# Kernel tuning notes

Measured on AMD Instinct MI355X. Metric: run time of the kernel, lower is better.

## Reference

```python
import jax, jax.numpy as jnp
import numpy as np

B, S, HID = 2, 2048, 4096
H, KVH, D = 32, 8, 128
EPS = 1e-6
BASE = 1000000.0


def _rmsnorm(x, w, eps=EPS):
    # x: [..., D]; RMSNorm over last dim with learned scale
    return x * jax.lax.rsqrt(jnp.mean(x * x, axis=-1, keepdims=True) + eps) * w


def _rope_interleaved(x, cos, sin):
    # x: [B, S, h, D]; cos/sin: [S, D//2]; is_neox_style=False (GPT-J interleaved pairs)
    x1 = x[..., 0::2]
    x2 = x[..., 1::2]
    c = cos[None, :, None, :]
    s = sin[None, :, None, :]
    o1 = x1 * c - x2 * s
    o2 = x2 * c + x1 * s
    return jnp.stack([o1, o2], axis=-1).reshape(x.shape)


def setup_inputs() -> dict:
    key = jax.random.key(0)
    ks = jax.random.split(key, 6)
    scale = 0.02
    return {
        "positions": jnp.arange(S, dtype=jnp.int32),
        "hidden_states": jax.random.normal(ks[0], (B, S, HID), jnp.float32),
        "Wq": jax.random.normal(ks[1], (HID, H * D), jnp.float32) * scale,
        "Wk": jax.random.normal(ks[2], (HID, KVH * D), jnp.float32) * scale,
        "Wv": jax.random.normal(ks[3], (HID, KVH * D), jnp.float32) * scale,
        "Wo": jax.random.normal(ks[4], (H * D, HID), jnp.float32) * scale,
        "q_norm_w": jnp.ones((D,), jnp.float32),
        "k_norm_w": jnp.ones((D,), jnp.float32),
    }


def reference(positions, hidden_states, Wq, Wk, Wv, Wo, q_norm_w, k_norm_w):
    # QKV projections (no bias)
    q = hidden_states @ Wq            # [B,S,H*D]
    k = hidden_states @ Wk            # [B,S,KVH*D]
    v = hidden_states @ Wv            # [B,S,KVH*D]

    # per-head QK RMSNorm
    q = _rmsnorm(q.reshape(B, S, H, D), q_norm_w)
    k = _rmsnorm(k.reshape(B, S, KVH, D), k_norm_w)
    v = v.reshape(B, S, KVH, D)

    # RoPE (non-neox / interleaved), rotary_dim == head_dim
    inv_freq = BASE ** (-jnp.arange(0, D, 2, dtype=jnp.float32) / D)  # [D/2]
    freqs = positions.astype(jnp.float32)[:, None] * inv_freq[None, :]  # [S, D/2]
    cos, sin = jnp.cos(freqs), jnp.sin(freqs)
    q = _rope_interleaved(q, cos, sin)
    k = _rope_interleaved(k, cos, sin)

    # GQA causal attention (prefill path of RadixAttention)
    rep = H // KVH
    kr = jnp.repeat(k, rep, axis=2)   # [B,S,H,D]
    vr = jnp.repeat(v, rep, axis=2)
    scores = jnp.einsum("bqhd,bkhd->bhqk", q, kr) * (D ** -0.5)
    causal = jnp.tril(jnp.ones((S, S), dtype=bool))
    scores = jnp.where(causal[None, None], scores, jnp.float32(-1e30))
    probs = jax.nn.softmax(scores, axis=-1)
    attn = jnp.einsum("bhqk,bkhd->bqhd", probs, vr).reshape(B, S, H * D)

    out = attn @ Wo                   # [B,S,HID]
    return out, k.reshape(B, S, KVH * D), v.reshape(B, S, KVH * D)
```

## Files before the change

### kernel.cpp

```cpp
#include <hip/hip_runtime.h>
#include <math.h>

#define B_SZ 2
#define S_LEN 2048
#define HID_D 4096
#define NH 32
#define NKV 8
#define HD 128
#define NTOK (B_SZ * S_LEN)

typedef short bf16x8 __attribute__((ext_vector_type(8)));
typedef float f32x4 __attribute__((ext_vector_type(4)));

__device__ inline unsigned short bf_rn(float f) {
    unsigned int u = __builtin_bit_cast(unsigned int, f);
    return (unsigned short)((u + 0x7FFFu + ((u >> 16) & 1u)) >> 16);
}
__device__ inline float bf_up(unsigned short s) {
    return __builtin_bit_cast(float, (unsigned int)s << 16);
}

__device__ inline void gload_lds16(const void* g, void* l) {
    __builtin_amdgcn_global_load_lds(
        (const __attribute__((address_space(1))) unsigned int*)g,
        (__attribute__((address_space(3))) unsigned int*)l, 16, 0, 0);
}

__global__ __launch_bounds__(64) void rope_table_kernel(const int* __restrict__ pos,
                                                        float* __restrict__ cosT,
                                                        float* __restrict__ sinT) {
    int s = blockIdx.x;
    int i = threadIdx.x;
    float p = (float)pos[s];
    float inv = expf((float)i * (-13.815510557964274f / 64.0f));
    float f = p * inv;
    cosT[s * 64 + i] = cosf(f);
    sinT[s * 64 + i] = sinf(f);
}

__global__ __launch_bounds__(256) void castv_kernel(const float* __restrict__ src,
                                                    unsigned short* __restrict__ dst,
                                                    int nquads) {
    int i = blockIdx.x * 256 + threadIdx.x;
    if (i >= nquads) return;
    float4 v = ((const float4*)src)[i];
    ushort4 o;
    o.x = bf_rn(v.x); o.y = bf_rn(v.y); o.z = bf_rn(v.z); o.w = bf_rn(v.w);
    ((ushort4*)dst)[i] = o;
}

__global__ __launch_bounds__(256) void cast_t_kernel(const float* __restrict__ src,
                                                     unsigned short* __restrict__ dst,
                                                     int K, int N) {
    __shared__ float tile[32][33];
    const int j0 = blockIdx.x << 5;
    const int i0 = blockIdx.y << 5;
    const int tx = threadIdx.x & 31, ty = threadIdx.x >> 5;
#pragma unroll
    for (int r = 0; r < 32; r += 8)
        tile[ty + r][tx] = src[(size_t)(i0 + ty + r) * N + j0 + tx];
    __syncthreads();
#pragma unroll
    for (int r = 0; r < 32; r += 8)
        dst[(size_t)(j0 + ty + r) * K + i0 + tx] = bf_rn(tile[tx][ty + r]);
}

__global__ __launch_bounds__(256) void vtrans_kernel(const float* __restrict__ vout,
                                                     unsigned short* __restrict__ vtb) {
    __shared__ float tile[32][33];
    const int bh = blockIdx.z;
    const int s0 = blockIdx.x << 5;
    const int d0 = blockIdx.y << 5;
    const int b = bh >> 3, kvh = bh & 7;
    const int tx = threadIdx.x & 31, ty = threadIdx.x >> 5;
#pragma unroll
    for (int r = 0; r < 32; r += 8)
        tile[ty + r][tx] = vout[((size_t)(b * S_LEN + s0 + ty + r) * NKV + kvh) * HD + d0 + tx];
    __syncthreads();
#pragma unroll
    for (int r = 0; r < 32; r += 8)
        vtb[((size_t)(b * NKV + kvh) * HD + d0 + ty + r) * S_LEN + s0 + tx] = bf_rn(tile[tx][ty + r]);
}

template <typename OUT>
__global__ __launch_bounds__(256) void gemm_bt_kernel(const unsigned short* __restrict__ A,
                                                      const unsigned short* __restrict__ Bt,
                                                      OUT* __restrict__ C,
                                                      int M, int N, int K) {
    __shared__ unsigned short As[128 * 32];
    __shared__ unsigned short Bs[128 * 32];
    const int t = threadIdx.x;
    const int lane = t & 63, w = t >> 6;
    const int wr = w >> 1, wc = w & 1;
    const int bm = blockIdx.y << 7, bn = blockIdx.x << 7;

    const int srow = w * 32 + (lane >> 2);
    const int skoff = (lane & 3) << 3;
    const unsigned short* aA0 = A + (size_t)(bm + srow) * K + skoff;
    const unsigned short* aA1 = aA0 + (size_t)16 * K;
    const unsigned short* aB0 = Bt + (size_t)(bn + srow) * K + skoff;
    const unsigned short* aB1 = aB0 + (size_t)16 * K;
    unsigned short* lA0 = As + (w * 2 + 0) * 512;
    unsigned short* lA1 = As + (w * 2 + 1) * 512;
    unsigned short* lB0 = Bs + (w * 2 + 0) * 512;
    unsigned short* lB1 = Bs + (w * 2 + 1) * 512;

    const int fr = lane & 15, fg = lane >> 4;
    const unsigned short* Asp = As + (wr * 64 + fr) * 32 + fg * 8;
    const unsigned short* Bsp = Bs + (wc * 64 + fr) * 32 + fg * 8;

    f32x4 acc[4][4];
#pragma unroll
    for (int m = 0; m < 4; ++m)
#pragma unroll
        for (int n = 0; n < 4; ++n) acc[m][n] = (f32x4)(0.0f);

    const int nk = K >> 5;
    for (int kc = 0; kc < nk; ++kc) {
        __syncthreads();
        const size_t go = (size_t)kc * 32;
        gload_lds16(aA0 + go, lA0);
        gload_lds16(aA1 + go, lA1);
        gload_lds16(aB0 + go, lB0);
        gload_lds16(aB1 + go, lB1);
        __syncthreads();

        bf16x8 af[4], bfr[4];
#pragma unroll
        for (int m = 0; m < 4; ++m) af[m] = *(const bf16x8*)(Asp + m * 512);
#pragma unroll
        for (int n = 0; n < 4; ++n) bfr[n] = *(const bf16x8*)(Bsp + n * 512);
#pragma unroll
        for (int m = 0; m < 4; ++m)
#pragma unroll
            for (int n = 0; n < 4; ++n)
                acc[m][n] = __builtin_amdgcn_mfma_f32_16x16x32_bf16(af[m], bfr[n], acc[m][n], 0, 0, 0);
    }

    const int crow = (lane >> 4) << 2, ccol = lane & 15;
#pragma unroll
    for (int m = 0; m < 4; ++m)
#pragma unroll
        for (int n = 0; n < 4; ++n) {
            OUT* Cp = C + (size_t)(bm + wr * 64 + m * 16 + crow) * N + bn + wc * 64 + n * 16 + ccol;
#pragma unroll
            for (int r = 0; r < 4; ++r) {
                float v = acc[m][n][r];
                if constexpr (sizeof(OUT) == 2) Cp[(size_t)r * N] = bf_rn(v);
                else                            Cp[(size_t)r * N] = v;
            }
        }
}

__global__ __launch_bounds__(64) void norm_rope_kernel(float* __restrict__ buf,
                                                       const float* __restrict__ w,
                                                       const float* __restrict__ cosT,
                                                       const float* __restrict__ sinT,
                                                       int nh) {
    int bid = blockIdx.x;
    int token = bid / nh;
    int h = bid - token * nh;
    int pos = token & (S_LEN - 1);
    int i = threadIdx.x;
    size_t base = (size_t)token * (nh * HD) + (size_t)h * HD + 2 * i;
    float2 x = *(const float2*)(buf + base);
    float ss = x.x * x.x + x.y * x.y;
#pragma unroll
    for (int off = 32; off > 0; off >>= 1) ss += __shfl_xor(ss, off);
    float rn = 1.0f / sqrtf(ss * (1.0f / 128.0f) + 1e-6f);
    float2 wv = *(const float2*)(w + 2 * i);
    float x1 = x.x * rn * wv.x;
    float x2 = x.y * rn * wv.y;
    float c = cosT[pos * 64 + i];
    float sn = sinT[pos * 64 + i];
    float2 o;
    o.x = x1 * c - x2 * sn;
    o.y = x2 * c + x1 * sn;
    *(float2*)(buf + base) = o;
}

__global__ __launch_bounds__(64) void norm_rope_bf16_kernel(unsigned short* __restrict__ buf,
                                                            const float* __restrict__ w,
                                                            const float* __restrict__ cosT,
                                                            const float* __restrict__ sinT,
                                                            int nh) {
    int bid = blockIdx.x;
    int token = bid / nh;
    int h = bid - token * nh;
    int pos = token & (S_LEN - 1);
    int i = threadIdx.x;
    size_t base = (size_t)token * (nh * HD) + (size_t)h * HD + 2 * i;
    unsigned int u = *(const unsigned int*)(buf + base);
    float x1 = bf_up((unsigned short)(u & 0xFFFFu));
    float x2 = bf_up((unsigned short)(u >> 16));
    float ss = x1 * x1 + x2 * x2;
#pragma unroll
    for (int off = 32; off > 0; off >>= 1) ss += __shfl_xor(ss, off);
    float rn = 1.0f / sqrtf(ss * (1.0f / 128.0f) + 1e-6f);
    float2 wv = *(const float2*)(w + 2 * i);
    x1 *= rn * wv.x;
    x2 *= rn * wv.y;
    float c = cosT[pos * 64 + i];
    float sn = sinT[pos * 64 + i];
    float o1 = x1 * c - x2 * sn;
    float o2 = x2 * c + x1 * sn;
    unsigned int ou = (unsigned int)bf_rn(o1) | ((unsigned int)bf_rn(o2) << 16);
    *(unsigned int*)(buf + base) = ou;
}

#define PADQ 136
#define PADV 72

__global__ __launch_bounds__(256) void attn_mfma_kernel(const unsigned short* __restrict__ Qb,
                                                        const float* __restrict__ Kf,
                                                        const unsigned short* __restrict__ Vb,
                                                        unsigned short* __restrict__ O) {
    __shared__ unsigned short Qs[64 * PADQ];
    __shared__ unsigned short Ks[64 * PADQ];
    __shared__ unsigned short Vt[128 * PADV];
    __shared__ unsigned short Ps[64 * PADV];
    const int t = threadIdx.x;
    const int lane = t & 63, w = t >> 6;
    const int c = lane & 15, g = lane >> 4;
    const int qt = blockIdx.x, h = blockIdx.y, b = blockIdx.z;
    const int kvh = h >> 2;
    const size_t tok0 = (size_t)b * S_LEN + (size_t)qt * 64;
    const size_t vbase = ((size_t)(b * NKV + kvh)) * HD * S_LEN;

    {
        const int r = t >> 2, c0 = (t & 3) * 32;
        const uint4* src = (const uint4*)(Qb + (tok0 + r) * HID_D + (size_t)h * HD + c0);
        uint4* dst = (uint4*)(Qs + r * PADQ + c0);
#pragma unroll
        for (int j = 0; j < 4; ++j) dst[j] = src[j];
    }
    __syncthreads();

    bf16x8 qf[4];
    {
        const unsigned short* qp = Qs + (w * 16 + c) * PADQ + g * 8;
#pragma unroll
        for (int ks = 0; ks < 4; ++ks) qf[ks] = *(const bf16x8*)(qp + ks * 32);
    }

    f32x4 o[8];
#pragma unroll
    for (int dt = 0; dt < 8; ++dt) o[dt] = (f32x4)(0.0f);
    float mrow[4], lrow[4];
#pragma unroll
    for (int r = 0; r < 4; ++r) { mrow[r] = -INFINITY; lrow[r] = 0.0f; }
    const float sc = 0.12751743f;

    for (int kt = 0; kt <= qt; ++kt) {
        __syncthreads();
        {
            const int r = t >> 2, c0 = (t & 3) * 32;
            const size_t gbase = ((size_t)b * S_LEN + (size_t)kt * 64 + r) * (NKV * HD) + (size_t)kvh * HD + c0;
            unsigned short* kd = Ks + r * PADQ + c0;
#pragma unroll
            for (int j = 0; j < 8; ++j) {
                float4 v = *(const float4*)(Kf + gbase + j * 4);
                ushort4 o4;
                o4.x = bf_rn(v.x); o4.y = bf_rn(v.y); o4.z = bf_rn(v.z); o4.w = bf_rn(v.w);
                *(ushort4*)(kd + j * 4) = o4;
            }
            const int vr = t >> 3;
            const int vc8 = (t & 7) * 8;
            const unsigned short* vsrc = Vb + vbase + (size_t)kt * 64 + vc8;
#pragma unroll
            for (int pp = 0; pp < 4; ++pp) {
                const int d = vr + pp * 32;
                *(uint4*)(Vt + d * PADV + vc8) = *(const uint4*)(vsrc + (size_t)d * S_LEN);
            }
        }
        __syncthreads();

        f32x4 s[4];
#pragma unroll
        for (int ct = 0; ct < 4; ++ct) s[ct] = (f32x4)(0.0f);
#pragma unroll
        for (int ks = 0; ks < 4; ++ks) {
            bf16x8 kf[4];
#pragma unroll
            for (int ct = 0; ct < 4; ++ct)
                kf[ct] = *(const bf16x8*)(Ks + (ct * 16 + c) * PADQ + ks * 32 + g * 8);
#pragma unroll
            for (int ct = 0; ct < 4; ++ct)
                s[ct] = __builtin_amdgcn_mfma_f32_16x16x32_bf16(qf[ks], kf[ct], s[ct], 0, 0, 0);
        }

        const int rowbase = qt * 64 + w * 16 + g * 4;
        const int colbase = kt * 64 + c;
#pragma unroll
        for (int r = 0; r < 4; ++r) {
            float v0 = s[0][r] * sc, v1 = s[1][r] * sc, v2 = s[2][r] * sc, v3 = s[3][r] * sc;
            if (kt == qt) {
                const int rq = rowbase + r;
                if (colbase + 0  > rq) v0 = -1e30f;
                if (colbase + 16 > rq) v1 = -1e30f;
                if (colbase + 32 > rq) v2 = -1e30f;
                if (colbase + 48 > rq) v3 = -1e30f;
            }
            float mx = fmaxf(fmaxf(v0, v1), fmaxf(v2, v3));
#pragma unroll
            for (int off = 8; off > 0; off >>= 1) mx = fmaxf(mx, __shfl_xor(mx, off));
            const float mn = fmaxf(mrow[r], mx);
            const float sf = exp2f(mrow[r] - mn);
            mrow[r] = mn;
            const float p0 = exp2f(v0 - mn), p1 = exp2f(v1 - mn);
            const float p2 = exp2f(v2 - mn), p3 = exp2f(v3 - mn);
            unsigned short* pr = Ps + (w * 16 + g * 4 + r) * PADV + c;
            pr[0]  = bf_rn(p0);
            pr[16] = bf_rn(p1);
            pr[32] = bf_rn(p2);
            pr[48] = bf_rn(p3);
            float rs = p0 + p1 + p2 + p3;
#pragma unroll
            for (int off = 8; off > 0; off >>= 1) rs += __shfl_xor(rs, off);
            lrow[r] = lrow[r] * sf + rs;
#pragma unroll
            for (int dt = 0; dt < 8; ++dt) o[dt][r] *= sf;
        }

#pragma unroll
        for (int ks = 0; ks < 2; ++ks) {
            bf16x8 pf = *(const bf16x8*)(Ps + (w * 16 + c) * PADV + ks * 32 + g * 8);
#pragma unroll
            for (int dt = 0; dt < 8; ++dt) {
                bf16x8 vf = *(const bf16x8*)(Vt + (dt * 16 + c) * PADV + ks * 32 + g * 8);
                o[dt] = __builtin_amdgcn_mfma_f32_16x16x32_bf16(pf, vf, o[dt], 0, 0, 0);
            }
        }
    }

#pragma unroll
    for (int r = 0; r < 4; ++r) {
        const float inv = 1.0f / lrow[r];
        const size_t rowoff = (tok0 + w * 16 + g * 4 + r) * HID_D + (size_t)h * HD;
#pragma unroll
        for (int dt = 0; dt < 8; ++dt)
            O[rowoff + dt * 16 + c] = bf_rn(o[dt][r] * inv);
    }
}

extern "C" void kernel_launch(void* const* d_in, const int* in_sizes, int n_in,
                              void* d_out, int out_size, void* d_ws, size_t ws_size,
                              hipStream_t stream) {
    const int* positions = (const int*)d_in[0];
    const float* hidden  = (const float*)d_in[1];
    const float* Wq      = (const float*)d_in[2];
    const float* Wk      = (const float*)d_in[3];
    const float* Wv      = (const float*)d_in[4];
    const float* Wo      = (const float*)d_in[5];
    const float* qw      = (const float*)d_in[6];
    const float* kw      = (const float*)d_in[7];

    float* out  = (float*)d_out;
    float* kout = out + (size_t)NTOK * HID_D;
    float* vout = kout + (size_t)NTOK * NKV * HD;

    char* w8 = (char*)d_ws;
    float* cosT = (float*)w8;
    float* sinT = cosT + S_LEN * 64;
    unsigned short* qbuf = (unsigned short*)(sinT + S_LEN * 64);
    unsigned short* hb   = qbuf + (size_t)NTOK * HID_D;
    unsigned short* Wt   = hb + (size_t)NTOK * HID_D;
    unsigned short* vtb  = Wt + (size_t)HID_D * HID_D;
    unsigned short* ab   = hb;

    rope_table_kernel<<<S_LEN, 64, 0, stream>>>(positions, cosT, sinT);
    castv_kernel<<<(NTOK * HID_D / 4 + 255) / 256, 256, 0, stream>>>(hidden, hb, NTOK * HID_D / 4);

    cast_t_kernel<<<dim3(NKV * HD / 32, HID_D / 32), 256, 0, stream>>>(Wk, Wt, HID_D, NKV * HD);
    gemm_bt_kernel<float><<<dim3(NKV * HD / 128, NTOK / 128), 256, 0, stream>>>(hb, Wt, kout, NTOK, NKV * HD, HID_D);
    cast_t_kernel<<<dim3(NKV * HD / 32, HID_D / 32), 256, 0, stream>>>(Wv, Wt, HID_D, NKV * HD);
    gemm_bt_kernel<float><<<dim3(NKV * HD / 128, NTOK / 128), 256, 0, stream>>>(hb, Wt, vout, NTOK, NKV * HD, HID_D);
    vtrans_kernel<<<dim3(S_LEN / 32, HD / 32, B_SZ * NKV), 256, 0, stream>>>(vout, vtb);
    cast_t_kernel<<<dim3(HID_D / 32, HID_D / 32), 256, 0, stream>>>(Wq, Wt, HID_D, HID_D);
    gemm_bt_kernel<unsigned short><<<dim3(HID_D / 128, NTOK / 128), 256, 0, stream>>>(hb, Wt, qbuf, NTOK, HID_D, HID_D);
    cast_t_kernel<<<dim3(HID_D / 32, HID_D / 32), 256, 0, stream>>>(Wo, Wt, HID_D, HID_D);

    norm_rope_bf16_kernel<<<NTOK * NH, 64, 0, stream>>>(qbuf, qw, cosT, sinT, NH);
    norm_rope_kernel<<<NTOK * NKV, 64, 0, stream>>>(kout, kw, cosT, sinT, NKV);

    attn_mfma_kernel<<<dim3(S_LEN / 64, NH, B_SZ), 256, 0, stream>>>(qbuf, kout, vtb, ab);

    gemm_bt_kernel<float><<<dim3(HID_D / 128, NTOK / 128), 256, 0, stream>>>(ab, Wt, out, NTOK, HID_D, HID_D);
}
```

Before: 1.364 ms.

## Prefetch next K tile into registers and share Q/K LDS buffer in attention

The attention kernel now loads the next K tile (fp32) into registers while the current tile's MFMA work runs, hiding global load latency. Q and K share one LDS buffer, which cuts shared memory per block, and launch_bounds now requests 4 blocks per SM for higher occupancy. The prefetch holds 32 extra floats per thread in registers, which may cause spills under the occupancy cap. The barrier is moved to the end of each iteration.

```diff
diff --git a/kernel.cpp b/kernel.cpp
--- a/kernel.cpp
+++ b/kernel.cpp
@@ -211,12 +211,11 @@
 #define PADQ 136
 #define PADV 72
 
-__global__ __launch_bounds__(256) void attn_mfma_kernel(const unsigned short* __restrict__ Qb,
-                                                        const float* __restrict__ Kf,
-                                                        const unsigned short* __restrict__ Vb,
-                                                        unsigned short* __restrict__ O) {
-    __shared__ unsigned short Qs[64 * PADQ];
-    __shared__ unsigned short Ks[64 * PADQ];
+__global__ __launch_bounds__(256, 4) void attn_mfma_kernel(const unsigned short* __restrict__ Qb,
+                                                           const float* __restrict__ Kf,
+                                                           const unsigned short* __restrict__ Vb,
+                                                           unsigned short* __restrict__ O) {
+    __shared__ unsigned short QKs[64 * PADQ];
     __shared__ unsigned short Vt[128 * PADV];
     __shared__ unsigned short Ps[64 * PADV];
     const int t = threadIdx.x;
@@ -230,7 +229,7 @@
     {
         const int r = t >> 2, c0 = (t & 3) * 32;
         const uint4* src = (const uint4*)(Qb + (tok0 + r) * HID_D + (size_t)h * HD + c0);
-        uint4* dst = (uint4*)(Qs + r * PADQ + c0);
+        uint4* dst = (uint4*)(QKs + r * PADQ + c0);
 #pragma unroll
         for (int j = 0; j < 4; ++j) dst[j] = src[j];
     }
@@ -238,9 +237,18 @@
 
     bf16x8 qf[4];
     {
-        const unsigned short* qp = Qs + (w * 16 + c) * PADQ + g * 8;
+        const unsigned short* qp = QKs + (w * 16 + c) * PADQ + g * 8;
 #pragma unroll
         for (int ks = 0; ks < 4; ++ks) qf[ks] = *(const bf16x8*)(qp + ks * 32);
+    }
+    __syncthreads();
+
+    const int kr_ = t >> 2, kc0 = (t & 3) * 32;
+    float4 kreg[8];
+    {
+        const size_t gb = ((size_t)b * S_LEN + 0 * 64 + kr_) * (NKV * HD) + (size_t)kvh * HD + kc0;
+#pragma unroll
+        for (int j = 0; j < 8; ++j) kreg[j] = *(const float4*)(Kf + gb + j * 4);
     }
 
     f32x4 o[8];
@@ -252,16 +260,13 @@
     const float sc = 0.12751743f;
 
     for (int kt = 0; kt <= qt; ++kt) {
-        __syncthreads();
         {
-            const int r = t >> 2, c0 = (t & 3) * 32;
-            const size_t gbase = ((size_t)b * S_LEN + (size_t)kt * 64 + r) * (NKV * HD) + (size_t)kvh * HD + c0;
-            unsigned short* kd = Ks + r * PADQ + c0;
+            unsigned short* kd = QKs + kr_ * PADQ + kc0;
 #pragma unroll
             for (int j = 0; j < 8; ++j) {
-                float4 v = *(const float4*)(Kf + gbase + j * 4);
                 ushort4 o4;
-                o4.x = bf_rn(v.x); o4.y = bf_rn(v.y); o4.z = bf_rn(v.z); o4.w = bf_rn(v.w);
+                o4.x = bf_rn(kreg[j].x); o4.y = bf_rn(kreg[j].y);
+                o4.z = bf_rn(kreg[j].z); o4.w = bf_rn(kreg[j].w);
                 *(ushort4*)(kd + j * 4) = o4;
             }
             const int vr = t >> 3;
@@ -275,6 +280,12 @@
         }
         __syncthreads();
 
+        if (kt < qt) {
+            const size_t gb = ((size_t)b * S_LEN + (size_t)(kt + 1) * 64 + kr_) * (NKV * HD) + (size_t)kvh * HD + kc0;
+#pragma unroll
+            for (int j = 0; j < 8; ++j) kreg[j] = *(const float4*)(Kf + gb + j * 4);
+        }
+
         f32x4 s[4];
 #pragma unroll
         for (int ct = 0; ct < 4; ++ct) s[ct] = (f32x4)(0.0f);
@@ -283,7 +294,7 @@
             bf16x8 kf[4];
 #pragma unroll
             for (int ct = 0; ct < 4; ++ct)
-                kf[ct] = *(const bf16x8*)(Ks + (ct * 16 + c) * PADQ + ks * 32 + g * 8);
+                kf[ct] = *(const bf16x8*)(QKs + (ct * 16 + c) * PADQ + ks * 32 + g * 8);
 #pragma unroll
             for (int ct = 0; ct < 4; ++ct)
                 s[ct] = __builtin_amdgcn_mfma_f32_16x16x32_bf16(qf[ks], kf[ct], s[ct], 0, 0, 0);
@@ -331,6 +342,7 @@
                 o[dt] = __builtin_amdgcn_mfma_f32_16x16x32_bf16(pf, vf, o[dt], 0, 0, 0);
             }
         }
+        __syncthreads();
     }
 
 #pragma unroll
```

Result: slower. 1.483 ms (+8.7%).

## Load Q and V fragments directly from global memory, drop LDS staging

Applied to the files above, without the earlier changes.

Q fragments are now read straight from global memory into registers, and the Q shared buffer and its barrier are removed. V fragments for the PV MFMA are likewise read directly from the transposed global V layout instead of being staged in LDS. The barrier is moved to just after the QK product, and the launch bounds now request 4 blocks per CU. The aim is to cut LDS footprint and staging traffic so occupancy rises, at the cost of uncoalesced, strided global loads for V (each lane reads 16 bytes across rows of length S_LEN) that depend on L2 for reuse.

```diff
diff --git a/kernel.cpp b/kernel.cpp
--- a/kernel.cpp
+++ b/kernel.cpp
@@ -211,13 +211,11 @@
 #define PADQ 136
 #define PADV 72
 
-__global__ __launch_bounds__(256) void attn_mfma_kernel(const unsigned short* __restrict__ Qb,
-                                                        const float* __restrict__ Kf,
-                                                        const unsigned short* __restrict__ Vb,
-                                                        unsigned short* __restrict__ O) {
-    __shared__ unsigned short Qs[64 * PADQ];
+__global__ __launch_bounds__(256, 4) void attn_mfma_kernel(const unsigned short* __restrict__ Qb,
+                                                           const float* __restrict__ Kf,
+                                                           const unsigned short* __restrict__ Vb,
+                                                           unsigned short* __restrict__ O) {
     __shared__ unsigned short Ks[64 * PADQ];
-    __shared__ unsigned short Vt[128 * PADV];
     __shared__ unsigned short Ps[64 * PADV];
     const int t = threadIdx.x;
     const int lane = t & 63, w = t >> 6;
@@ -227,20 +225,11 @@
     const size_t tok0 = (size_t)b * S_LEN + (size_t)qt * 64;
     const size_t vbase = ((size_t)(b * NKV + kvh)) * HD * S_LEN;
 
-    {
-        const int r = t >> 2, c0 = (t & 3) * 32;
-        const uint4* src = (const uint4*)(Qb + (tok0 + r) * HID_D + (size_t)h * HD + c0);
-        uint4* dst = (uint4*)(Qs + r * PADQ + c0);
-#pragma unroll
-        for (int j = 0; j < 4; ++j) dst[j] = src[j];
-    }
-    __syncthreads();
-
     bf16x8 qf[4];
     {
-        const unsigned short* qp = Qs + (w * 16 + c) * PADQ + g * 8;
-#pragma unroll
-        for (int ks = 0; ks < 4; ++ks) qf[ks] = *(const bf16x8*)(qp + ks * 32);
+        const unsigned short* qrow = Qb + (tok0 + w * 16 + c) * HID_D + (size_t)h * HD;
+#pragma unroll
+        for (int ks = 0; ks < 4; ++ks) qf[ks] = *(const bf16x8*)(qrow + ks * 32 + g * 8);
     }
 
     f32x4 o[8];
@@ -251,27 +240,20 @@
     for (int r = 0; r < 4; ++r) { mrow[r] = -INFINITY; lrow[r] = 0.0f; }
     const float sc = 0.12751743f;
 
+    const int kr_ = t >> 2, kc0 = (t & 3) * 32;
+
     for (int kt = 0; kt <= qt; ++kt) {
-        __syncthreads();
         {
-            const int r = t >> 2, c0 = (t & 3) * 32;
-            const size_t gbase = ((size_t)b * S_LEN + (size_t)kt * 64 + r) * (NKV * HD) + (size_t)kvh * HD + c0;
-            unsigned short* kd = Ks + r * PADQ + c0;
+            const size_t gb = ((size_t)b * S_LEN + (size_t)kt * 64 + kr_) * (NKV * HD) + (size_t)kvh * HD + kc0;
+            unsigned short* kd = Ks + kr_ * PADQ + kc0;
 #pragma unroll
             for (int j = 0; j < 8; ++j) {
-                float4 v = *(const float4*)(Kf + gbase + j * 4);
+                float4 v = *(const float4*)(Kf + gb + j * 4);
                 ushort4 o4;
-                o4.x = bf_rn(v.x); o4.y = bf_rn(v.y); o4.z = bf_rn(v.z); o4.w = bf_rn(v.w);
+                o4.x = bf_rn(v.x); o4.y = bf_rn(v.y);
+                o4.z = bf_rn(v.z); o4.w = bf_rn(v.w);
                 *(ushort4*)(kd + j * 4) = o4;
             }
-            const int vr = t >> 3;
-            const int vc8 = (t & 7) * 8;
-            const unsigned short* vsrc = Vb + vbase + (size_t)kt * 64 + vc8;
-#pragma unroll
-            for (int pp = 0; pp < 4; ++pp) {
-                const int d = vr + pp * 32;
-                *(uint4*)(Vt + d * PADV + vc8) = *(const uint4*)(vsrc + (size_t)d * S_LEN);
-            }
         }
         __syncthreads();
 
@@ -288,6 +270,7 @@
             for (int ct = 0; ct < 4; ++ct)
                 s[ct] = __builtin_amdgcn_mfma_f32_16x16x32_bf16(qf[ks], kf[ct], s[ct], 0, 0, 0);
         }
+        __syncthreads();
 
         const int rowbase = qt * 64 + w * 16 + g * 4;
         const int colbase = kt * 64 + c;
@@ -322,12 +305,13 @@
             for (int dt = 0; dt < 8; ++dt) o[dt][r] *= sf;
         }
 
+        const unsigned short* vt0 = Vb + vbase + (size_t)kt * 64 + g * 8;
 #pragma unroll
         for (int ks = 0; ks < 2; ++ks) {
             bf16x8 pf = *(const bf16x8*)(Ps + (w * 16 + c) * PADV + ks * 32 + g * 8);
 #pragma unroll
             for (int dt = 0; dt < 8; ++dt) {
-                bf16x8 vf = *(const bf16x8*)(Vt + (dt * 16 + c) * PADV + ks * 32 + g * 8);
+                bf16x8 vf = *(const bf16x8*)(vt0 + (size_t)(dt * 16 + c) * S_LEN + ks * 32);
                 o[dt] = __builtin_amdgcn_mfma_f32_16x16x32_bf16(pf, vf, o[dt], 0, 0, 0);
             }
         }
```

Result: slower. 1.569 ms (+15.0%).
